# Kernel tuning notes

Measured on AMD Instinct MI355X. Metric: run time of the kernel, lower is better.

The kernel has to match this reference:

```python
import jax, jax.numpy as jnp
import numpy as np

N_NODES = 50000
NEG_SLOPE = 0.2
EPS = 1e-16


def _gat_conv(x, src, dst, W, a_src, a_dst, bias, heads, out_c, concat):
    """PyG-style GATConv (self-loops assumed already added to src/dst)."""
    N = x.shape[0]
    h = (x @ W).reshape(N, heads, out_c)                 # [N,H,C]
    s_src = jnp.sum(h * a_src, axis=-1)                  # [N,H]
    s_dst = jnp.sum(h * a_dst, axis=-1)                  # [N,H]
    e = jax.nn.leaky_relu(s_src[src] + s_dst[dst], NEG_SLOPE)  # [E,H]
    # segment softmax over incoming edges of each dst node
    m = jax.ops.segment_max(e, dst, num_segments=N)      # [N,H]
    e = jnp.exp(e - m[dst])
    z = jax.ops.segment_sum(e, dst, num_segments=N)      # [N,H]
    alpha = e / (z[dst] + EPS)                           # [E,H]
    out = jax.ops.segment_sum(h[src] * alpha[:, :, None], dst, num_segments=N)  # [N,H,C]
    if concat:
        out = out.reshape(N, heads * out_c)
    else:
        out = out.mean(axis=1)
    return out + bias


def setup_inputs() -> dict:
    key = jax.random.key(0)
    ks = jax.random.split(key, 12)
    N, E, nfeat, nhid, nclass = N_NODES, 800000, 512, 256, 40
    heads, head_dim = 4, nhid // 4
    g = lambda k, shape, fan: (jax.random.normal(k, shape, jnp.float32) * (1.0 / np.sqrt(fan)))
    return {
        "x": jax.random.normal(ks[0], (N, nfeat), jnp.float32),
        "adj": jax.random.randint(ks[1], (2, E), 0, N, jnp.int64),
        "W1": g(ks[2], (nfeat, heads * head_dim), nfeat),
        "att_src1": g(ks[3], (heads, head_dim), head_dim),
        "att_dst1": g(ks[4], (heads, head_dim), head_dim),
        "b1": jnp.zeros((heads * head_dim,), jnp.float32),
        "W2": g(ks[5], (nhid, nclass), nhid),
        "att_src2": g(ks[6], (1, nclass), nclass),
        "att_dst2": g(ks[7], (1, nclass), nclass),
        "b2": jnp.zeros((nclass,), jnp.float32),
    }


def reference(x, adj, W1, att_src1, att_dst1, b1, W2, att_src2, att_dst2, b2):
    N = x.shape[0]
    loops = jnp.arange(N, dtype=adj.dtype)
    src = jnp.concatenate([adj[0], loops])   # PyG GATConv add_self_loops=True
    dst = jnp.concatenate([adj[1], loops])
    h = _gat_conv(x, src, dst, W1, att_src1, att_dst1, b1, heads=4, out_c=64, concat=True)
    h = jax.nn.relu(h)
    # dropout: eval mode => identity
    out = _gat_conv(h, src, dst, W2, att_src2, att_dst2, b2, heads=1, out_c=40, concat=False)
    return out
```

## Files before the change

### kernel.cpp

```cpp
#include <hip/hip_runtime.h>
#include <hip/hip_bf16.h>
#include <math.h>

#define NFEAT 512
#define NHID 256
#define HEADS 4
#define HDIM 64
#define NCLASS 40
#define NEG_SLOPE 0.2f
#define EPS_Z 1e-16f

typedef short bf16x8 __attribute__((ext_vector_type(8)));
typedef float f32x4 __attribute__((ext_vector_type(4)));

__device__ __forceinline__ float lrelu(float x) {
  return x > 0.f ? x : NEG_SLOPE * x;
}

__device__ __forceinline__ ushort f2bf(float f) {
  union { float f; uint u; } c; c.f = f;
  uint u = c.u;
  uint r = u + 0x7FFFu + ((u >> 16) & 1u);
  return (ushort)(r >> 16);
}
__device__ __forceinline__ float bf2f(ushort h) {
  union { uint u; float f; } c; c.u = ((uint)h) << 16;
  return c.f;
}

__device__ __forceinline__ uint cvtpk(float lo, float hi) {
  uint r;
  asm("v_cvt_pk_bf16_f32 %0, %1, %2" : "=v"(r) : "v"(lo), "v"(hi));
  return r;
}


__global__ void count_kernel(const int* __restrict__ dstv, int E, int* __restrict__ counts) {
  int i = blockIdx.x * blockDim.x + threadIdx.x;
  if (i < E) atomicAdd(&counts[dstv[i]], 1);
}

__global__ __launch_bounds__(1024) void scan_a(const int* __restrict__ counts,
    int* __restrict__ excl, int* __restrict__ bsum, int n) {
  __shared__ int tmp[1024];
  int t = threadIdx.x;
  int i = blockIdx.x * 1024 + t;
  int v = (i < n) ? counts[i] : 0;
  tmp[t] = v;
  __syncthreads();
  for (int off = 1; off < 1024; off <<= 1) {
    int u = (t >= off) ? tmp[t - off] : 0;
    __syncthreads();
    tmp[t] += u;
    __syncthreads();
  }
  if (i < n) excl[i] = tmp[t] - v;
  if (t == 1023) bsum[blockIdx.x] = tmp[t];
}

__global__ __launch_bounds__(1024) void scan_b(int* __restrict__ bsum, int nb) {
  __shared__ int tmp[1024];
  int t = threadIdx.x;
  tmp[t] = (t < nb) ? bsum[t] : 0;
  __syncthreads();
  for (int off = 1; off < 1024; off <<= 1) {
    int u = (t >= off) ? tmp[t - off] : 0;
    __syncthreads();
    tmp[t] += u;
    __syncthreads();
  }
  if (t < nb) bsum[t] = tmp[t];
}

__global__ void scan_c(const int* __restrict__ excl, const int* __restrict__ bsum_incl,
    int* __restrict__ row_off, int* __restrict__ cursor, int n, int E) {
  int i = blockIdx.x * blockDim.x + threadIdx.x;
  if (i < n) {
    int b = i >> 10;
    int off = (b > 0) ? bsum_incl[b - 1] : 0;
    int v = excl[i] + off;
    row_off[i] = v;
    cursor[i] = v;
  }
  if (i == 0) row_off[n] = E;
}

__global__ void scatter_kernel(const int* __restrict__ srcv, const int* __restrict__ dstv,
                               int E, int* __restrict__ cursor, int* __restrict__ edge_src) {
  int i = blockIdx.x * blockDim.x + threadIdx.x;
  if (i < E) {
    int pos = atomicAdd(&cursor[dstv[i]], 1);
    edge_src[pos] = srcv[i];
  }
}


__global__ __launch_bounds__(64) void wprep_kernel(const float* __restrict__ W,
    ushort* __restrict__ Bh) {
  int fb = blockIdx.x;
  int ct = fb >> 4, ks = fb & 15;
  int l = threadIdx.x;
  int g = l >> 4, rr = l & 15;
  uint hw[4];
  #pragma unroll
  for (int p = 0; p < 4; ++p) {
    ushort h2v[2];
    #pragma unroll
    for (int q = 0; q < 2; ++q) {
      int e = p * 2 + q;
      int k = ks * 32 + 4 * g + (e & 3) + 16 * (e >> 2);
      int col = ct * 16 + rr;
      h2v[q] = f2bf(W[k * NHID + col]);
    }
    hw[p] = (uint)h2v[0] | ((uint)h2v[1] << 16);
  }
  size_t o = ((size_t)fb * 64 + l) * 8;
  uint4 hv; hv.x = hw[0]; hv.y = hw[1]; hv.z = hw[2]; hv.w = hw[3];
  *(uint4*)&Bh[o] = hv;
}


__global__ __launch_bounds__(256, 4) void gemm1_mfma(const float* __restrict__ A,
    const ushort* __restrict__ Bh,
    const float* __restrict__ asrc, const float* __restrict__ adst,
    ushort* __restrict__ h1b, float* __restrict__ ssrc1, float* __restrict__ sdst1,
    int M) {
  __shared__ float A_s[2][64 * 64];
  const int tid = threadIdx.x;
  const int lane = tid & 63;
  const int wc = tid >> 6;
  const int g = lane >> 4, rr = lane & 15;
  const int row0 = blockIdx.x * 64;

  f32x4 acc[4][4] = {};

  auto stage = [&](int ki, int buf) {
    #pragma unroll
    for (int j = 0; j < 4; ++j) {
      int grp = wc * 4 + j;
      int s = grp * 64 + lane;
      int r = s >> 4;
      int us = s & 15;
      int ud = us ^ (r & 7);
      int gr = row0 + r;
      if (gr >= M) gr = M - 1;
      const float* src = &A[(size_t)gr * NFEAT + ki * 64 + ud * 4];
      float* dst = &A_s[buf][grp * 256];
      __builtin_amdgcn_global_load_lds(
          (const __attribute__((address_space(1))) float*)src,
          (__attribute__((address_space(3))) float*)dst, 16, 0, 0);
    }
  };

  stage(0, 0);
  __syncthreads();

  for (int ki = 0; ki < 8; ++ki) {
    const int cur = ki & 1;
    if (ki < 7) stage(ki + 1, cur ^ 1);

    #pragma unroll
    for (int kk = 0; kk < 2; ++kk) {
      const int ks = ki * 2 + kk;
      bf16x8 bhf[4];
      #pragma unroll
      for (int ni = 0; ni < 4; ++ni) {
        int ct = wc * 4 + ni;
        size_t bidx = ((size_t)(ct * 16 + ks) * 64 + lane) * 8;
        bhf[ni] = *(const bf16x8*)&Bh[bidx];
      }
      #pragma unroll
      for (int mi = 0; mi < 4; ++mi) {
        int row = mi * 16 + rr;
        int u0 = (8 * kk + g) ^ (row & 7);
        int u1 = (8 * kk + 4 + g) ^ (row & 7);
        f32x4 lo = *(const f32x4*)&A_s[cur][row * 64 + u0 * 4];
        f32x4 hi = *(const f32x4*)&A_s[cur][row * 64 + u1 * 4];
        uint w0 = cvtpk(lo[0], lo[1]);
        uint w1 = cvtpk(lo[2], lo[3]);
        uint w2 = cvtpk(hi[0], hi[1]);
        uint w3 = cvtpk(hi[2], hi[3]);
        union { uint u[4]; bf16x8 v; } af;
        af.u[0] = w0; af.u[1] = w1; af.u[2] = w2; af.u[3] = w3;
        #pragma unroll
        for (int ni = 0; ni < 4; ++ni) {
          acc[mi][ni] = __builtin_amdgcn_mfma_f32_16x16x32_bf16(af.v, bhf[ni], acc[mi][ni], 0, 0, 0);
        }
      }
    }
    __syncthreads();
  }

  float a_s[4], a_d[4];
  #pragma unroll
  for (int ni = 0; ni < 4; ++ni) {
    a_s[ni] = asrc[wc * 64 + ni * 16 + rr];
    a_d[ni] = adst[wc * 64 + ni * 16 + rr];
  }

  #pragma unroll
  for (int mi = 0; mi < 4; ++mi) {
    #pragma unroll
    for (int j = 0; j < 4; ++j) {
      int r = row0 + mi * 16 + g * 4 + j;
      bool ok = r < M;
      float ps = 0.f, pd = 0.f;
      #pragma unroll
      for (int ni = 0; ni < 4; ++ni) {
        float v = acc[mi][ni][j];
        ps += v * a_s[ni];
        pd += v * a_d[ni];
        if (ok) h1b[(size_t)r * NHID + wc * 64 + ni * 16 + rr] = f2bf(v);
      }
      #pragma unroll
      for (int m = 1; m < 16; m <<= 1) {
        ps += __shfl_xor(ps, m, 64);
        pd += __shfl_xor(pd, m, 64);
      }
      if (ok && rr == 0) {
        ssrc1[r * HEADS + wc] = ps;
        sdst1[r * HEADS + wc] = pd;
      }
    }
  }
}


__global__ __launch_bounds__(256) void gemm2_fused(const ushort* __restrict__ A,
    const float* __restrict__ B, const float* __restrict__ asrc,
    const float* __restrict__ adst, ushort* __restrict__ h2b,
    float* __restrict__ ssrc2, float* __restrict__ sdst2, int M) {
  __shared__ float As[16][64 + 1];
  __shared__ float Bs[16][68];
  const int tid = threadIdx.x;
  const int tx = tid & 15, ty = tid >> 4;
  const int row0 = blockIdx.x * 64;
  float acc[4][4] = {};

  const int la_r = tid >> 2;
  const int la_k = (tid & 3) * 4;
  const int lb_r = tid >> 4;
  const int lb_c = (tid & 15) * 4;

  for (int k0 = 0; k0 < NHID; k0 += 16) {
    float a0 = 0.f, a1 = 0.f, a2 = 0.f, a3 = 0.f;
    int ar = row0 + la_r;
    if (ar < M) {
      ushort4 uv = *(const ushort4*)&A[(size_t)ar * NHID + k0 + la_k];
      a0 = bf2f(uv.x); a1 = bf2f(uv.y); a2 = bf2f(uv.z); a3 = bf2f(uv.w);
    }
    As[la_k + 0][la_r] = a0;
    As[la_k + 1][la_r] = a1;
    As[la_k + 2][la_r] = a2;
    As[la_k + 3][la_r] = a3;

    float4 bv = make_float4(0.f, 0.f, 0.f, 0.f);
    const float* Brow = &B[(size_t)(k0 + lb_r) * NCLASS];
    if (lb_c + 3 < NCLASS) bv = *(const float4*)&Brow[lb_c];
    *(float4*)&Bs[lb_r][lb_c] = bv;
    __syncthreads();

    #pragma unroll
    for (int k = 0; k < 16; ++k) {
      float x0 = As[k][ty * 4 + 0];
      float x1 = As[k][ty * 4 + 1];
      float x2 = As[k][ty * 4 + 2];
      float x3 = As[k][ty * 4 + 3];
      float4 b = *(const float4*)&Bs[k][tx * 4];
      acc[0][0] += x0 * b.x; acc[0][1] += x0 * b.y; acc[0][2] += x0 * b.z; acc[0][3] += x0 * b.w;
      acc[1][0] += x1 * b.x; acc[1][1] += x1 * b.y; acc[1][2] += x1 * b.z; acc[1][3] += x1 * b.w;
      acc[2][0] += x2 * b.x; acc[2][1] += x2 * b.y; acc[2][2] += x2 * b.z; acc[2][3] += x2 * b.w;
      acc[3][0] += x3 * b.x; acc[3][1] += x3 * b.y; acc[3][2] += x3 * b.z; acc[3][3] += x3 * b.w;
    }
    __syncthreads();
  }

  const int cbase = tx * 4;
  const bool cok = cbase + 3 < NCLASS;
  float4 av_s = make_float4(0.f, 0.f, 0.f, 0.f);
  float4 av_d = make_float4(0.f, 0.f, 0.f, 0.f);
  if (cok) {
    av_s = *(const float4*)&asrc[cbase];
    av_d = *(const float4*)&adst[cbase];
  }

  #pragma unroll
  for (int i = 0; i < 4; ++i) {
    int r = row0 + ty * 4 + i;
    bool ok = r < M;
    float ps = acc[i][0] * av_s.x + acc[i][1] * av_s.y + acc[i][2] * av_s.z + acc[i][3] * av_s.w;
    float pd = acc[i][0] * av_d.x + acc[i][1] * av_d.y + acc[i][2] * av_d.z + acc[i][3] * av_d.w;
    #pragma unroll
    for (int m = 1; m < 16; m <<= 1) {
      ps += __shfl_xor(ps, m, 64);
      pd += __shfl_xor(pd, m, 64);
    }
    if (ok && cok) {
      ushort4 o;
      o.x = f2bf(acc[i][0]); o.y = f2bf(acc[i][1]);
      o.z = f2bf(acc[i][2]); o.w = f2bf(acc[i][3]);
      *(ushort4*)&h2b[(size_t)r * NCLASS + cbase] = o;
    }
    if (ok && tx == 0) { ssrc2[r] = ps; sdst2[r] = pd; }
  }
}


__global__ __launch_bounds__(64) void agg1_kernel(const ushort* __restrict__ h1b,
    const float* __restrict__ s_src, const float* __restrict__ s_dst,
    const int* __restrict__ row_off, const int* __restrict__ edge_src,
    const float* __restrict__ b1, ushort* __restrict__ hrelu_b) {
  int v = blockIdx.x;
  int l = threadIdx.x;
  int head = l >> 4;
  int elane = l & 15;
  int c = l * 4;
  float sdv = s_dst[v * HEADS + head];

  float wself = __expf(lrelu(s_src[v * HEADS + head] + sdv));
  ushort4 hv = *(const ushort4*)&h1b[(size_t)v * NHID + c];
  float4 acc = make_float4(wself * bf2f(hv.x), wself * bf2f(hv.y),
                           wself * bf2f(hv.z), wself * bf2f(hv.w));
  float zp = (elane == 0) ? wself : 0.f;

  int i = row_off[v], end = row_off[v + 1];
  for (; i < end; i += 16) {
    int cnt = end - i;
    if (cnt > 16) cnt = 16;
    bool val = elane < cnt;
    int u = edge_src[val ? (i + elane) : i];
    float wl = 0.f;
    if (val) wl = __expf(lrelu(s_src[u * HEADS + head] + sdv));
    zp += wl;

    int e = 0;
    for (; e + 3 < cnt; e += 4) {
      int u0 = __shfl(u, e + 0);
      int u1 = __shfl(u, e + 1);
      int u2 = __shfl(u, e + 2);
      int u3 = __shfl(u, e + 3);
      float w0 = __shfl(wl, (l & 48) | (e + 0));
      float w1 = __shfl(wl, (l & 48) | (e + 1));
      float w2 = __shfl(wl, (l & 48) | (e + 2));
      float w3 = __shfl(wl, (l & 48) | (e + 3));
      ushort4 r0 = *(const ushort4*)&h1b[(size_t)u0 * NHID + c];
      ushort4 r1 = *(const ushort4*)&h1b[(size_t)u1 * NHID + c];
      ushort4 r2 = *(const ushort4*)&h1b[(size_t)u2 * NHID + c];
      ushort4 r3 = *(const ushort4*)&h1b[(size_t)u3 * NHID + c];
      acc.x += w0 * bf2f(r0.x) + w1 * bf2f(r1.x) + w2 * bf2f(r2.x) + w3 * bf2f(r3.x);
      acc.y += w0 * bf2f(r0.y) + w1 * bf2f(r1.y) + w2 * bf2f(r2.y) + w3 * bf2f(r3.y);
      acc.z += w0 * bf2f(r0.z) + w1 * bf2f(r1.z) + w2 * bf2f(r2.z) + w3 * bf2f(r3.z);
      acc.w += w0 * bf2f(r0.w) + w1 * bf2f(r1.w) + w2 * bf2f(r2.w) + w3 * bf2f(r3.w);
    }
    for (; e < cnt; ++e) {
      int ue = __shfl(u, e);
      float we = __shfl(wl, (l & 48) | e);
      ushort4 ru = *(const ushort4*)&h1b[(size_t)ue * NHID + c];
      acc.x += we * bf2f(ru.x);
      acc.y += we * bf2f(ru.y);
      acc.z += we * bf2f(ru.z);
      acc.w += we * bf2f(ru.w);
    }
  }
  #pragma unroll
  for (int m = 1; m < 16; m <<= 1) zp += __shfl_xor(zp, m, 64);

  float inv = 1.f / (zp + EPS_Z);
  float4 bb = *(const float4*)&b1[c];
  ushort4 o;
  o.x = f2bf(fmaxf(acc.x * inv + bb.x, 0.f));
  o.y = f2bf(fmaxf(acc.y * inv + bb.y, 0.f));
  o.z = f2bf(fmaxf(acc.z * inv + bb.z, 0.f));
  o.w = f2bf(fmaxf(acc.w * inv + bb.w, 0.f));
  *(ushort4*)&hrelu_b[(size_t)v * NHID + c] = o;
}

__global__ __launch_bounds__(64) void agg2_kernel(const ushort* __restrict__ h2b,
    const float* __restrict__ s_src, const float* __restrict__ s_dst,
    const int* __restrict__ row_off, const int* __restrict__ edge_src,
    const float* __restrict__ b2, float* __restrict__ out) {
  int v = blockIdx.x;
  int l = threadIdx.x;
  bool act = l < NCLASS;
  float sdv = s_dst[v];

  float wself = __expf(lrelu(s_src[v] + sdv));
  float acc = act ? wself * bf2f(h2b[(size_t)v * NCLASS + l]) : 0.f;
  float zp = (l == 0) ? wself : 0.f;

  int i = row_off[v], end = row_off[v + 1];
  for (; i < end; i += 64) {
    int cnt = end - i;
    if (cnt > 64) cnt = 64;
    bool val = l < cnt;
    int u = edge_src[val ? (i + l) : i];
    float wl = 0.f;
    if (val) wl = __expf(lrelu(s_src[u] + sdv));
    zp += wl;

    int e = 0;
    for (; e + 3 < cnt; e += 4) {
      int u0 = __shfl(u, e + 0);
      int u1 = __shfl(u, e + 1);
      int u2 = __shfl(u, e + 2);
      int u3 = __shfl(u, e + 3);
      float w0 = __shfl(wl, e + 0);
      float w1 = __shfl(wl, e + 1);
      float w2 = __shfl(wl, e + 2);
      float w3 = __shfl(wl, e + 3);
      ushort p0 = 0, p1 = 0, p2 = 0, p3 = 0;
      if (act) {
        p0 = h2b[(size_t)u0 * NCLASS + l];
        p1 = h2b[(size_t)u1 * NCLASS + l];
        p2 = h2b[(size_t)u2 * NCLASS + l];
        p3 = h2b[(size_t)u3 * NCLASS + l];
      }
      if (act) acc += w0 * bf2f(p0) + w1 * bf2f(p1) + w2 * bf2f(p2) + w3 * bf2f(p3);
    }
    for (; e < cnt; ++e) {
      int ue = __shfl(u, e);
      float we = __shfl(wl, e);
      if (act) acc += we * bf2f(h2b[(size_t)ue * NCLASS + l]);
    }
  }
  #pragma unroll
  for (int m = 1; m < 64; m <<= 1) zp += __shfl_xor(zp, m, 64);

  if (act) out[(size_t)v * NCLASS + l] = acc / (zp + EPS_Z) + b2[l];
}


extern "C" void kernel_launch(void* const* d_in, const int* in_sizes, int n_in,
                              void* d_out, int out_size, void* d_ws, size_t ws_size,
                              hipStream_t stream) {
  const float* x   = (const float*)d_in[0];
  const int*   adj = (const int*)d_in[1];
  const float* W1  = (const float*)d_in[2];
  const float* as1 = (const float*)d_in[3];
  const float* ad1 = (const float*)d_in[4];
  const float* b1  = (const float*)d_in[5];
  const float* W2  = (const float*)d_in[6];
  const float* as2 = (const float*)d_in[7];
  const float* ad2 = (const float*)d_in[8];
  const float* b2  = (const float*)d_in[9];
  float* out = (float*)d_out;

  const int N = in_sizes[0] / NFEAT;
  const int E = in_sizes[1] / 2;

  char* ws = (char*)d_ws;
  size_t off = 0;
  auto alloc = [&](size_t bytes) -> void* {
    void* p = ws + off;
    off = (off + bytes + 255) & ~(size_t)255;
    return p;
  };
  ushort* h1b    = (ushort*)alloc((size_t)N * NHID * 2);
  ushort* hrelub = (ushort*)alloc((size_t)N * NHID * 2);
  ushort* h2b    = (ushort*)alloc((size_t)N * NCLASS * 2);
  float* ssrc1   = (float*)alloc((size_t)N * HEADS * 4);
  float* sdst1   = (float*)alloc((size_t)N * HEADS * 4);
  float* ssrc2   = (float*)alloc((size_t)N * 4);
  float* sdst2   = (float*)alloc((size_t)N * 4);
  int* counts    = (int*)alloc((size_t)N * 4);
  int* cursor    = (int*)alloc((size_t)N * 4);
  int* row_off   = (int*)alloc((size_t)(N + 1) * 4);
  int* edge_src  = (int*)alloc((size_t)E * 4);
  int* excl      = (int*)alloc((size_t)N * 4);
  int* bsum      = (int*)alloc((size_t)1024 * 4);
  ushort* whp    = (ushort*)alloc((size_t)NFEAT * NHID * 2);
  (void)ws_size;

  const int* srcv = adj;
  const int* dstv = adj + E;
  const int nb = (N + 1023) / 1024;

  wprep_kernel<<<256, 64, 0, stream>>>(W1, whp);

  hipMemsetAsync(counts, 0, (size_t)N * 4, stream);
  count_kernel<<<(E + 255) / 256, 256, 0, stream>>>(dstv, E, counts);
  scan_a<<<nb, 1024, 0, stream>>>(counts, excl, bsum, N);
  scan_b<<<1, 1024, 0, stream>>>(bsum, nb);
  scan_c<<<(N + 255) / 256, 256, 0, stream>>>(excl, bsum, row_off, cursor, N, E);
  scatter_kernel<<<(E + 255) / 256, 256, 0, stream>>>(srcv, dstv, E, cursor, edge_src);

  gemm1_mfma<<<(N + 63) / 64, 256, 0, stream>>>(x, whp, as1, ad1, h1b, ssrc1, sdst1, N);
  agg1_kernel<<<N, 64, 0, stream>>>(h1b, ssrc1, sdst1, row_off, edge_src, b1, hrelub);

  gemm2_fused<<<(N + 63) / 64, 256, 0, stream>>>(hrelub, W2, as2, ad2, h2b, ssrc2, sdst2, N);
  agg2_kernel<<<N, 64, 0, stream>>>(h2b, ssrc2, sdst2, row_off, edge_src, b2, out);
}
```

Measured before the change: 268.9 us.

## Fuse CSR construction into a single cooperative kernel with grid syncs

Replaces the memset, count, three-stage scan and scatter kernels with one cooperative kernel that uses grid-wide syncs between phases. This removes several kernel launches and the intermediate excl buffer, cutting launch and dependency overhead in CSR building. The kernel uses 256 blocks of 1024 threads and assumes N fits in 256*1024 per-block chunks. Grid syncs cost something, and the lower parallelism in the atomic phases may slow the count and scatter steps.

```diff
diff --git a/kernel.cpp b/kernel.cpp
--- a/kernel.cpp
+++ b/kernel.cpp
@@ -1,6 +1,9 @@
 #include <hip/hip_runtime.h>
 #include <hip/hip_bf16.h>
+#include <hip/hip_cooperative_groups.h>
 #include <math.h>
+
+namespace cg = cooperative_groups;
 
 #define NFEAT 512
 #define NHID 256
@@ -10,6 +13,9 @@
 #define NEG_SLOPE 0.2f
 #define EPS_Z 1e-16f
 
+#define CSR_BLOCKS 256
+#define CSR_THREADS 1024
+
 typedef short bf16x8 __attribute__((ext_vector_type(8)));
 typedef float f32x4 __attribute__((ext_vector_type(4)));
 
@@ -35,60 +41,63 @@
 }
 
 
-__global__ void count_kernel(const int* __restrict__ dstv, int E, int* __restrict__ counts) {
-  int i = blockIdx.x * blockDim.x + threadIdx.x;
-  if (i < E) atomicAdd(&counts[dstv[i]], 1);
-}
-
-__global__ __launch_bounds__(1024) void scan_a(const int* __restrict__ counts,
-    int* __restrict__ excl, int* __restrict__ bsum, int n) {
-  __shared__ int tmp[1024];
-  int t = threadIdx.x;
-  int i = blockIdx.x * 1024 + t;
-  int v = (i < n) ? counts[i] : 0;
-  tmp[t] = v;
+__global__ __launch_bounds__(1024) void csr_kernel(
+    const int* __restrict__ srcv, const int* __restrict__ dstv, int N, int E,
+    int* __restrict__ counts, int* __restrict__ row_off, int* __restrict__ cursor,
+    int* __restrict__ edge_src, int* __restrict__ bsum) {
+  cg::grid_group grid = cg::this_grid();
+  const int t = threadIdx.x;
+  const int gid = blockIdx.x * blockDim.x + t;
+  const int gstride = gridDim.x * blockDim.x;
+
+  for (int i = gid; i < N; i += gstride) counts[i] = 0;
+  grid.sync();
+
+  for (int i = gid; i < E; i += gstride) atomicAdd(&counts[dstv[i]], 1);
+  grid.sync();
+
+  __shared__ int tmp[CSR_THREADS];
+  const int C = (N + gridDim.x - 1) / gridDim.x;
+  const int b0 = blockIdx.x * C;
+  int vcnt = 0;
+  if (t < C && b0 + t < N) vcnt = counts[b0 + t];
+  tmp[t] = vcnt;
   __syncthreads();
-  for (int off = 1; off < 1024; off <<= 1) {
+  for (int off = 1; off < CSR_THREADS; off <<= 1) {
     int u = (t >= off) ? tmp[t - off] : 0;
     __syncthreads();
     tmp[t] += u;
     __syncthreads();
   }
-  if (i < n) excl[i] = tmp[t] - v;
-  if (t == 1023) bsum[blockIdx.x] = tmp[t];
-}
-
-__global__ __launch_bounds__(1024) void scan_b(int* __restrict__ bsum, int nb) {
-  __shared__ int tmp[1024];
-  int t = threadIdx.x;
-  tmp[t] = (t < nb) ? bsum[t] : 0;
-  __syncthreads();
-  for (int off = 1; off < 1024; off <<= 1) {
-    int u = (t >= off) ? tmp[t - off] : 0;
+  if (t == CSR_THREADS - 1) bsum[blockIdx.x] = tmp[t];
+  const int excl_t = tmp[t] - vcnt;
+  grid.sync();
+
+  if (blockIdx.x == 0) {
+    int nb = gridDim.x;
+    int vb = (t < nb) ? bsum[t] : 0;
+    tmp[t] = vb;
     __syncthreads();
-    tmp[t] += u;
-    __syncthreads();
-  }
-  if (t < nb) bsum[t] = tmp[t];
-}
-
-__global__ void scan_c(const int* __restrict__ excl, const int* __restrict__ bsum_incl,
-    int* __restrict__ row_off, int* __restrict__ cursor, int n, int E) {
-  int i = blockIdx.x * blockDim.x + threadIdx.x;
-  if (i < n) {
-    int b = i >> 10;
-    int off = (b > 0) ? bsum_incl[b - 1] : 0;
-    int v = excl[i] + off;
-    row_off[i] = v;
-    cursor[i] = v;
-  }
-  if (i == 0) row_off[n] = E;
-}
-
-__global__ void scatter_kernel(const int* __restrict__ srcv, const int* __restrict__ dstv,
-                               int E, int* __restrict__ cursor, int* __restrict__ edge_src) {
-  int i = blockIdx.x * blockDim.x + threadIdx.x;
-  if (i < E) {
+    for (int off = 1; off < CSR_THREADS; off <<= 1) {
+      int u = (t >= off) ? tmp[t - off] : 0;
+      __syncthreads();
+      tmp[t] += u;
+      __syncthreads();
+    }
+    if (t < nb) bsum[t] = tmp[t];
+  }
+  grid.sync();
+
+  const int boff = (blockIdx.x > 0) ? bsum[blockIdx.x - 1] : 0;
+  if (t < C && b0 + t < N) {
+    int val = excl_t + boff;
+    row_off[b0 + t] = val;
+    cursor[b0 + t] = val;
+  }
+  if (gid == 0) row_off[N] = E;
+  grid.sync();
+
+  for (int i = gid; i < E; i += gstride) {
     int pos = atomicAdd(&cursor[dstv[i]], 1);
     edge_src[pos] = srcv[i];
   }
@@ -445,8 +454,8 @@
   const float* b2  = (const float*)d_in[9];
   float* out = (float*)d_out;
 
-  const int N = in_sizes[0] / NFEAT;
-  const int E = in_sizes[1] / 2;
+  int N = in_sizes[0] / NFEAT;
+  int E = in_sizes[1] / 2;
 
   char* ws = (char*)d_ws;
   size_t off = 0;
@@ -466,23 +475,22 @@
   int* cursor    = (int*)alloc((size_t)N * 4);
   int* row_off   = (int*)alloc((size_t)(N + 1) * 4);
   int* edge_src  = (int*)alloc((size_t)E * 4);
-  int* excl      = (int*)alloc((size_t)N * 4);
   int* bsum      = (int*)alloc((size_t)1024 * 4);
   ushort* whp    = (ushort*)alloc((size_t)NFEAT * NHID * 2);
   (void)ws_size;
 
   const int* srcv = adj;
   const int* dstv = adj + E;
-  const int nb = (N + 1023) / 1024;
 
   wprep_kernel<<<256, 64, 0, stream>>>(W1, whp);
 
-  hipMemsetAsync(counts, 0, (size_t)N * 4, stream);
-  count_kernel<<<(E + 255) / 256, 256, 0, stream>>>(dstv, E, counts);
-  scan_a<<<nb, 1024, 0, stream>>>(counts, excl, bsum, N);
-  scan_b<<<1, 1024, 0, stream>>>(bsum, nb);
-  scan_c<<<(N + 255) / 256, 256, 0, stream>>>(excl, bsum, row_off, cursor, N, E);
-  scatter_kernel<<<(E + 255) / 256, 256, 0, stream>>>(srcv, dstv, E, cursor, edge_src);
+  {
+    void* args[] = {(void*)&srcv, (void*)&dstv, (void*)&N, (void*)&E,
+                    (void*)&counts, (void*)&row_off, (void*)&cursor,
+                    (void*)&edge_src, (void*)&bsum};
+    hipLaunchCooperativeKernel((void*)csr_kernel, dim3(CSR_BLOCKS),
+                               dim3(CSR_THREADS), args, 0, stream);
+  }
 
   gemm1_mfma<<<(N + 63) / 64, 256, 0, stream>>>(x, whp, as1, ad1, h1b, ssrc1, sdst1, N);
   agg1_kernel<<<N, 64, 0, stream>>>(h1b, ssrc1, sdst1, row_off, edge_src, b1, hrelub);
```

After: 400.0 us. 48.8% more time.
